# Kernel optimization log

Measured on AMD Instinct MI355X. Metric: run time of the kernel, lower is better.

Reference implementation:

```python
import jax, jax.numpy as jnp
import numpy as np

DIM = 64
HEADS = 4
N_NODES = 50000
N_EDGES = 800000
NEG_SLOPE = 0.2


def setup_inputs() -> dict:
    key = jax.random.key(0)
    k1, k2, k3, k4, k5 = jax.random.split(key, 5)
    meta_x = jax.random.normal(k1, (N_NODES, DIM), dtype=jnp.float32)
    meta_edge_index = jax.random.randint(k2, (2, N_EDGES), 0, N_NODES, dtype=jnp.int64)
    # GATConv params: shared source/dest Linear (no bias), per-head attention vecs, output bias.
    glorot = float(np.sqrt(2.0 / (DIM + HEADS * DIM)))
    W = jax.random.normal(k3, (DIM, HEADS * DIM), dtype=jnp.float32) * glorot  # x @ W
    att_src = jax.random.normal(k4, (1, HEADS, DIM), dtype=jnp.float32) * glorot
    att_dst = jax.random.normal(k5, (1, HEADS, DIM), dtype=jnp.float32) * glorot
    bias = jnp.zeros((DIM,), dtype=jnp.float32)
    return {"meta_x": meta_x, "meta_edge_index": meta_edge_index,
            "W": W, "att_src": att_src, "att_dst": att_dst, "bias": bias}


def reference(meta_x, meta_edge_index, W, att_src, att_dst, bias):
    N = meta_x.shape[0]
    # PyG GATConv default: add self-loops
    loops = jnp.arange(N, dtype=meta_edge_index.dtype)
    edge = jnp.concatenate([meta_edge_index, jnp.stack([loops, loops])], axis=1)
    src, dst = edge[0], edge[1]

    x = (meta_x @ W).reshape(N, HEADS, DIM)            # [N, H, C]
    a_src = jnp.sum(x * att_src, axis=-1)              # [N, H]
    a_dst = jnp.sum(x * att_dst, axis=-1)              # [N, H]

    logits = a_src[src] + a_dst[dst]                   # [E, H]
    logits = jax.nn.leaky_relu(logits, NEG_SLOPE)

    # segment softmax over edges grouped by destination node
    seg_max = jax.ops.segment_max(logits, dst, num_segments=N)   # [N, H]
    ex = jnp.exp(logits - seg_max[dst])
    seg_sum = jax.ops.segment_sum(ex, dst, num_segments=N)
    alpha = ex / (seg_sum[dst] + 1e-16)                # [E, H]

    msg = x[src] * alpha[:, :, None]                   # [E, H, C]
    out = jax.ops.segment_sum(msg, dst, num_segments=N)  # [N, H, C]
    # concat=False -> mean over heads, then bias
    return out.mean(axis=1) + bias
```

## Files before the change

kernel.cpp:

```cpp
#include <hip/hip_runtime.h>
#include <hip/hip_bf16.h>
#include <math.h>

#define MAXDEG 64

__device__ __forceinline__ float lrelu(float v) { return v > 0.0f ? v : 0.2f * v; }

__global__ void prep_kernel(int4* __restrict__ cnt4, int n4,
                            const float* __restrict__ W, const float* __restrict__ att_src,
                            const float* __restrict__ att_dst, float* __restrict__ wsrc,
                            float* __restrict__ wdst) {
  int idx = blockIdx.x * 256 + threadIdx.x;
  for (int i = idx; i < n4; i += gridDim.x * 256) cnt4[i] = make_int4(0, 0, 0, 0);
  if (blockIdx.x == 0) {
    int t = threadIdx.x;
    int h = t >> 6, k = t & 63;
    const float* wrow = W + (size_t)k * 256 + h * 64;
    const float* as = att_src + h * 64;
    const float* ad = att_dst + h * 64;
    float ss = 0.f, sd = 0.f;
#pragma unroll
    for (int c = 0; c < 64; ++c) {
      float w = wrow[c];
      ss = fmaf(w, as[c], ss);
      sd = fmaf(w, ad[c], sd);
    }
    wsrc[k * 4 + h] = ss;
    wdst[k * 4 + h] = sd;
  }
}

__global__ void nh_kernel(const float* __restrict__ x, const float4* __restrict__ wsrc4,
                          const float4* __restrict__ wdst4, float4* __restrict__ asrc4,
                          float4* __restrict__ adst4, __hip_bfloat16* __restrict__ xh,
                          const int* __restrict__ ei, int* __restrict__ counts,
                          int E, int N, int nbh) {
  if (blockIdx.x < nbh) {
    int i = blockIdx.x * 256 + threadIdx.x;
    int E4 = E >> 2;
    if (i < E4) {
      int4 d = ((const int4*)(ei + E))[i];
      atomicAdd(&counts[d.x], 1);
      atomicAdd(&counts[d.y], 1);
      atomicAdd(&counts[d.z], 1);
      atomicAdd(&counts[d.w], 1);
    } else if (i < E4 + N) {
      atomicAdd(&counts[i - E4], 1);
    }
    return;
  }
  int lane = threadIdx.x & 63;
  int n = (blockIdx.x - nbh) * 4 + (threadIdx.x >> 6);
  if (n >= N) return;
  float xv = x[(size_t)n * 64 + lane];
  xh[(size_t)n * 64 + lane] = __float2bfloat16(xv);
  float4 ws = wsrc4[lane], wd = wdst4[lane];
  float s0 = xv * ws.x, s1 = xv * ws.y, s2 = xv * ws.z, s3 = xv * ws.w;
  float d0 = xv * wd.x, d1 = xv * wd.y, d2 = xv * wd.z, d3 = xv * wd.w;
#pragma unroll
  for (int m = 1; m < 64; m <<= 1) {
    s0 += __shfl_xor(s0, m, 64); s1 += __shfl_xor(s1, m, 64);
    s2 += __shfl_xor(s2, m, 64); s3 += __shfl_xor(s3, m, 64);
    d0 += __shfl_xor(d0, m, 64); d1 += __shfl_xor(d1, m, 64);
    d2 += __shfl_xor(d2, m, 64); d3 += __shfl_xor(d3, m, 64);
  }
  if (lane == 0) {
    asrc4[n] = make_float4(s0, s1, s2, s3);
    adst4[n] = make_float4(d0, d1, d2, d3);
  }
}

__global__ void nattn_kernel(const float* __restrict__ x, const float4* __restrict__ wsrc4,
                             const float4* __restrict__ wdst4, float4* __restrict__ asrc4,
                             float4* __restrict__ adst4, __hip_bfloat16* __restrict__ xh,
                             int N) {
  int lane = threadIdx.x & 63;
  int n = blockIdx.x * 4 + (threadIdx.x >> 6);
  if (n >= N) return;
  float xv = x[(size_t)n * 64 + lane];
  xh[(size_t)n * 64 + lane] = __float2bfloat16(xv);
  float4 ws = wsrc4[lane], wd = wdst4[lane];
  float s0 = xv * ws.x, s1 = xv * ws.y, s2 = xv * ws.z, s3 = xv * ws.w;
  float d0 = xv * wd.x, d1 = xv * wd.y, d2 = xv * wd.z, d3 = xv * wd.w;
#pragma unroll
  for (int m = 1; m < 64; m <<= 1) {
    s0 += __shfl_xor(s0, m, 64); s1 += __shfl_xor(s1, m, 64);
    s2 += __shfl_xor(s2, m, 64); s3 += __shfl_xor(s3, m, 64);
    d0 += __shfl_xor(d0, m, 64); d1 += __shfl_xor(d1, m, 64);
    d2 += __shfl_xor(d2, m, 64); d3 += __shfl_xor(d3, m, 64);
  }
  if (lane == 0) {
    asrc4[n] = make_float4(s0, s1, s2, s3);
    adst4[n] = make_float4(d0, d1, d2, d3);
  }
}

__global__ void hist_kernel(const int* __restrict__ ei, int* __restrict__ counts,
                            int E, int N) {
  int e = blockIdx.x * 256 + threadIdx.x;
  int ET = E + N;
  if (e >= ET) return;
  int dst = (e < E) ? ei[(size_t)E + e] : (e - E);
  atomicAdd(&counts[dst], 1);
}

__global__ void scatter_kernel(const int* __restrict__ ei, int* __restrict__ cursor,
                               int* __restrict__ src_sorted, int E, int N) {
  int e = blockIdx.x * 256 + threadIdx.x;
  int ET = E + N;
  if (e >= ET) return;
  int src, dst;
  if (e < E) {
    src = ei[e];
    dst = ei[(size_t)E + e];
  } else {
    src = dst = e - E;
  }
  int pos = atomicAdd(&cursor[dst], 1);
  src_sorted[pos] = src;
}

__global__ void scatter8_kernel(const int* __restrict__ ei, int* __restrict__ cursor,
                                int* __restrict__ srt, int E, int N) {
  int slice = blockIdx.x & 7;
  int bid = blockIdx.x >> 3;
  int nb = gridDim.x >> 3;
  int chunk = (N + 7) >> 3;
  int lo = slice * chunk;
  int hi = lo + chunk; if (hi > N) hi = N;
  int E4 = E >> 2;
  const int4* s4p = (const int4*)ei;
  const int4* d4p = (const int4*)(ei + E);
  int stride = nb * 256;
  for (int i = bid * 256 + threadIdx.x; i < E4; i += stride) {
    int4 d4 = d4p[i];
    bool bx = (d4.x >= lo && d4.x < hi), by = (d4.y >= lo && d4.y < hi);
    bool bz = (d4.z >= lo && d4.z < hi), bw = (d4.w >= lo && d4.w < hi);
    if (!(bx || by || bz || bw)) continue;
    int4 s4 = s4p[i];
    if (bx) { int p = atomicAdd(&cursor[d4.x], 1); srt[p] = s4.x; }
    if (by) { int p = atomicAdd(&cursor[d4.y], 1); srt[p] = s4.y; }
    if (bz) { int p = atomicAdd(&cursor[d4.z], 1); srt[p] = s4.z; }
    if (bw) { int p = atomicAdd(&cursor[d4.w], 1); srt[p] = s4.w; }
  }
  for (int n = lo + bid * 256 + threadIdx.x; n < hi; n += stride) {
    int p = atomicAdd(&cursor[n], 1);
    srt[p] = n;
  }
}

__global__ void scanABC_kernel(const int* __restrict__ cnt, int* __restrict__ row,
                               int* __restrict__ cur, int N, int ntiles) {
  __shared__ int tl[256];
  __shared__ int part[256];
  int b = blockIdx.x, t = threadIdx.x;
  int s = 0;
  if (t < ntiles) {
    const int4* c4 = (const int4*)cnt + t * 64;
    for (int i = 0; i < 64; ++i) {
      int4 v = c4[i];
      s += v.x + v.y + v.z + v.w;
    }
  }
  tl[t] = s;
  __syncthreads();
  for (int d = 1; d < 256; d <<= 1) {
    int u = (t >= d) ? tl[t - d] : 0;
    __syncthreads();
    tl[t] += u;
    __syncthreads();
  }
  int tileoff = (b == 0) ? 0 : tl[b - 1];
  int idx = b * 256 + t;
  int c = (idx < N) ? cnt[idx] : 0;
  part[t] = c;
  __syncthreads();
  for (int d = 1; d < 256; d <<= 1) {
    int u = (t >= d) ? part[t - d] : 0;
    __syncthreads();
    part[t] += u;
    __syncthreads();
  }
  int exc = part[t] - c + tileoff;
  if (idx < N) {
    row[idx] = exc;
    cur[idx] = exc;
    if (idx == N - 1) row[N] = exc + c;
  }
}

__global__ void scanA_kernel(const int* __restrict__ cnt, int* __restrict__ tsum, int N) {
  int b = blockIdx.x, t = threadIdx.x;
  int idx = b * 256 + t;
  int v = (idx < N) ? cnt[idx] : 0;
#pragma unroll
  for (int m = 1; m < 64; m <<= 1) v += __shfl_xor(v, m, 64);
  __shared__ int ws[4];
  if ((t & 63) == 0) ws[t >> 6] = v;
  __syncthreads();
  if (t == 0) tsum[b] = ws[0] + ws[1] + ws[2] + ws[3];
}

__global__ void scanB_kernel(int* __restrict__ tsum, int ntiles) {
  __shared__ int part[256];
  int t = threadIdx.x;
  int carry = 0;
  for (int b0 = 0; b0 < ntiles; b0 += 256) {
    int idx = b0 + t;
    int v = (idx < ntiles) ? tsum[idx] : 0;
    part[t] = v;
    __syncthreads();
    for (int d = 1; d < 256; d <<= 1) {
      int u = (t >= d) ? part[t - d] : 0;
      __syncthreads();
      part[t] += u;
      __syncthreads();
    }
    if (idx < ntiles) tsum[idx] = part[t] - v + carry;
    carry += part[255];
    __syncthreads();
  }
}

__global__ void scanC_kernel(const int* __restrict__ cnt, const int* __restrict__ tsum,
                             int* __restrict__ row, int* __restrict__ cur, int N) {
  __shared__ int part[256];
  int b = blockIdx.x, t = threadIdx.x;
  int idx = b * 256 + t;
  int c = (idx < N) ? cnt[idx] : 0;
  part[t] = c;
  __syncthreads();
  for (int d = 1; d < 256; d <<= 1) {
    int u = (t >= d) ? part[t - d] : 0;
    __syncthreads();
    part[t] += u;
    __syncthreads();
  }
  int exc = part[t] - c + tsum[b];
  if (idx < N) {
    row[idx] = exc;
    cur[idx] = exc;
    if (idx == N - 1) row[N] = exc + c;
  }
}

__global__ __launch_bounds__(256) void agg_kernel(
    const int* __restrict__ srt, const int* __restrict__ row,
    const float4* __restrict__ asrc4, const float4* __restrict__ adst4,
    const __hip_bfloat16* __restrict__ xh, __hip_bfloat16* __restrict__ agg, int N) {
  __shared__ float4 alL[4][MAXDEG];
  __shared__ int slL[4][MAXDEG];
  int t = threadIdx.x, w = t >> 6, lane = t & 63;
  int n = blockIdx.x * 4 + w;
  if (n >= N) return;
  int start = row[n], end = row[n + 1];
  int deg = end - start;
  float4 ad = adst4[n];
  float t0 = 0.f, t1 = 0.f, t2 = 0.f, t3 = 0.f;
  if (deg <= MAXDEG) {
    for (int b = 0; b < deg; b += 64) {
      if (b + lane < deg) {
        int sl = srt[start + b + lane];
        float4 as = asrc4[sl];
        float4 e;
        e.x = __expf(lrelu(as.x + ad.x));
        e.y = __expf(lrelu(as.y + ad.y));
        e.z = __expf(lrelu(as.z + ad.z));
        e.w = __expf(lrelu(as.w + ad.w));
        alL[w][b + lane] = e;
        slL[w][b + lane] = sl;
        t0 += e.x; t1 += e.y; t2 += e.z; t3 += e.w;
      }
    }
  } else {
    for (int b = start; b < end; b += 64) {
      int idx = b + lane;
      if (idx < end) {
        int sl = srt[idx];
        float4 as = asrc4[sl];
        t0 += __expf(lrelu(as.x + ad.x));
        t1 += __expf(lrelu(as.y + ad.y));
        t2 += __expf(lrelu(as.z + ad.z));
        t3 += __expf(lrelu(as.w + ad.w));
      }
    }
  }
#pragma unroll
  for (int m = 1; m < 64; m <<= 1) {
    t0 += __shfl_xor(t0, m, 64);
    t1 += __shfl_xor(t1, m, 64);
    t2 += __shfl_xor(t2, m, 64);
    t3 += __shfl_xor(t3, m, 64);
  }
  float r0 = 0.25f / (t0 + 1e-16f), r1 = 0.25f / (t1 + 1e-16f);
  float r2 = 0.25f / (t2 + 1e-16f), r3 = 0.25f / (t3 + 1e-16f);
  float a0 = 0.f, a1 = 0.f, a2 = 0.f, a3 = 0.f;
  if (deg <= MAXDEG) {
    int j = 0;
    for (; j + 4 <= deg; j += 4) {
      float4 e0 = alL[w][j], e1 = alL[w][j + 1], e2 = alL[w][j + 2], e3 = alL[w][j + 3];
      int q0 = slL[w][j], q1 = slL[w][j + 1], q2 = slL[w][j + 2], q3 = slL[w][j + 3];
      float v0 = __bfloat162float(xh[(size_t)q0 * 64 + lane]);
      float v1 = __bfloat162float(xh[(size_t)q1 * 64 + lane]);
      float v2 = __bfloat162float(xh[(size_t)q2 * 64 + lane]);
      float v3 = __bfloat162float(xh[(size_t)q3 * 64 + lane]);
      a0 = fmaf(e0.x, v0, a0); a1 = fmaf(e0.y, v0, a1);
      a2 = fmaf(e0.z, v0, a2); a3 = fmaf(e0.w, v0, a3);
      a0 = fmaf(e1.x, v1, a0); a1 = fmaf(e1.y, v1, a1);
      a2 = fmaf(e1.z, v1, a2); a3 = fmaf(e1.w, v1, a3);
      a0 = fmaf(e2.x, v2, a0); a1 = fmaf(e2.y, v2, a1);
      a2 = fmaf(e2.z, v2, a2); a3 = fmaf(e2.w, v2, a3);
      a0 = fmaf(e3.x, v3, a0); a1 = fmaf(e3.y, v3, a1);
      a2 = fmaf(e3.z, v3, a2); a3 = fmaf(e3.w, v3, a3);
    }
    for (; j < deg; ++j) {
      float4 e0 = alL[w][j];
      int q0 = slL[w][j];
      float v0 = __bfloat162float(xh[(size_t)q0 * 64 + lane]);
      a0 = fmaf(e0.x, v0, a0); a1 = fmaf(e0.y, v0, a1);
      a2 = fmaf(e0.z, v0, a2); a3 = fmaf(e0.w, v0, a3);
    }
  } else {
    for (int b = start; b < end; b += 64) {
      int cnt = end - b;
      if (cnt > 64) cnt = 64;
      int idx = b + lane;
      int sl = 0;
      float e0 = 0.f, e1 = 0.f, e2 = 0.f, e3 = 0.f;
      if (idx < end) {
        sl = srt[idx];
        float4 as = asrc4[sl];
        e0 = __expf(lrelu(as.x + ad.x));
        e1 = __expf(lrelu(as.y + ad.y));
        e2 = __expf(lrelu(as.z + ad.z));
        e3 = __expf(lrelu(as.w + ad.w));
      }
      for (int j = 0; j < cnt; ++j) {
        int sj = __shfl(sl, j, 64);
        float b0 = __shfl(e0, j, 64), b1 = __shfl(e1, j, 64);
        float b2 = __shfl(e2, j, 64), b3 = __shfl(e3, j, 64);
        float v = __bfloat162float(xh[(size_t)sj * 64 + lane]);
        a0 = fmaf(b0, v, a0); a1 = fmaf(b1, v, a1);
        a2 = fmaf(b2, v, a2); a3 = fmaf(b3, v, a3);
      }
    }
  }
  __hip_bfloat16* ao = agg + (size_t)n * 256;
  ao[lane] = __float2bfloat16(a0 * r0);
  ao[64 + lane] = __float2bfloat16(a1 * r1);
  ao[128 + lane] = __float2bfloat16(a2 * r2);
  ao[192 + lane] = __float2bfloat16(a3 * r3);
}

__global__ __launch_bounds__(256) void proj_kernel(
    const __hip_bfloat16* __restrict__ agg, const float* __restrict__ W,
    const float* __restrict__ bias, float* __restrict__ out, int N) {
  __shared__ float aggL[4][256];
  __shared__ float pL[4][4][64];
  int t = threadIdx.x, w = t >> 6, lane = t & 63;
  float Wreg[64];
#pragma unroll
  for (int k = 0; k < 64; ++k) Wreg[k] = W[(size_t)k * 256 + w * 64 + lane];
  float bv = bias[lane];
  int ngroups = (N + 3) >> 2;
  for (int g = blockIdx.x; g < ngroups; g += gridDim.x) {
    int n0 = g * 4;
    __syncthreads();
    {
      int nn = n0 + w;
      if (nn < N) {
        ushort4 u = ((const ushort4*)(agg + (size_t)nn * 256))[t & 63];
        float4 f;
        f.x = __bfloat162float(*(__hip_bfloat16*)&u.x);
        f.y = __bfloat162float(*(__hip_bfloat16*)&u.y);
        f.z = __bfloat162float(*(__hip_bfloat16*)&u.z);
        f.w = __bfloat162float(*(__hip_bfloat16*)&u.w);
        *(float4*)&aggL[w][(t & 63) * 4] = f;
      } else {
        *(float4*)&aggL[w][(t & 63) * 4] = make_float4(0.f, 0.f, 0.f, 0.f);
      }
    }
    __syncthreads();
    float acc0 = 0.f, acc1 = 0.f, acc2 = 0.f, acc3 = 0.f;
#pragma unroll
    for (int k4 = 0; k4 < 16; ++k4) {
      float4 av0 = *(const float4*)&aggL[0][w * 64 + k4 * 4];
      float4 av1 = *(const float4*)&aggL[1][w * 64 + k4 * 4];
      float4 av2 = *(const float4*)&aggL[2][w * 64 + k4 * 4];
      float4 av3 = *(const float4*)&aggL[3][w * 64 + k4 * 4];
      float w0 = Wreg[k4 * 4 + 0], w1 = Wreg[k4 * 4 + 1];
      float w2 = Wreg[k4 * 4 + 2], w3 = Wreg[k4 * 4 + 3];
      acc0 = fmaf(av0.x, w0, acc0); acc0 = fmaf(av0.y, w1, acc0);
      acc0 = fmaf(av0.z, w2, acc0); acc0 = fmaf(av0.w, w3, acc0);
      acc1 = fmaf(av1.x, w0, acc1); acc1 = fmaf(av1.y, w1, acc1);
      acc1 = fmaf(av1.z, w2, acc1); acc1 = fmaf(av1.w, w3, acc1);
      acc2 = fmaf(av2.x, w0, acc2); acc2 = fmaf(av2.y, w1, acc2);
      acc2 = fmaf(av2.z, w2, acc2); acc2 = fmaf(av2.w, w3, acc2);
      acc3 = fmaf(av3.x, w0, acc3); acc3 = fmaf(av3.y, w1, acc3);
      acc3 = fmaf(av3.z, w2, acc3); acc3 = fmaf(av3.w, w3, acc3);
    }
    pL[w][0][lane] = acc0;
    pL[w][1][lane] = acc1;
    pL[w][2][lane] = acc2;
    pL[w][3][lane] = acc3;
    __syncthreads();
    int nn = n0 + w;
    if (nn < N) {
      out[(size_t)nn * 64 + lane] = pL[0][w][lane] + pL[1][w][lane] +
                                    pL[2][w][lane] + pL[3][w][lane] + bv;
    }
  }
}

extern "C" void kernel_launch(void* const* d_in, const int* in_sizes, int n_in,
                              void* d_out, int out_size, void* d_ws, size_t ws_size,
                              hipStream_t stream) {
  const float* meta_x = (const float*)d_in[0];
  const int* ei = (const int*)d_in[1];
  const float* W = (const float*)d_in[2];
  const float* att_src = (const float*)d_in[3];
  const float* att_dst = (const float*)d_in[4];
  const float* bias = (const float*)d_in[5];
  float* out = (float*)d_out;

  int N = in_sizes[0] / 64;
  int E = in_sizes[1] / 2;
  int ET = E + N;
  int ntiles = (N + 255) / 256;

  char* ws = (char*)d_ws;
  size_t off = 0;
  auto alloc = [&](size_t bytes) {
    size_t o = off;
    off += (bytes + 255) & ~(size_t)255;
    return o;
  };
  size_t o_wsrc = alloc(64 * 4 * sizeof(float));
  size_t o_wdst = alloc(64 * 4 * sizeof(float));
  size_t o_asrc = alloc((size_t)N * 4 * sizeof(float));
  size_t o_adst = alloc((size_t)N * 4 * sizeof(float));
  size_t o_cnt = alloc((size_t)ntiles * 256 * sizeof(int));
  size_t o_row = alloc(((size_t)N + 1) * sizeof(int));
  size_t o_cur = alloc((size_t)N * sizeof(int));
  size_t o_srt = alloc((size_t)ET * sizeof(int));
  size_t o_ts = alloc((size_t)ntiles * sizeof(int));
  size_t o_xh = alloc((size_t)N * 64 * sizeof(__hip_bfloat16));
  size_t o_agg = alloc((size_t)N * 256 * sizeof(__hip_bfloat16));
  bool split = (ws_size >= off);
  (void)split;

  float* wsrc = (float*)(ws + o_wsrc);
  float* wdst = (float*)(ws + o_wdst);
  float4* asrc4 = (float4*)(ws + o_asrc);
  float4* adst4 = (float4*)(ws + o_adst);
  int* cnt = (int*)(ws + o_cnt);
  int* row = (int*)(ws + o_row);
  int* cur = (int*)(ws + o_cur);
  int* srt = (int*)(ws + o_srt);
  int* tsum = (int*)(ws + o_ts);
  __hip_bfloat16* xh = (__hip_bfloat16*)(ws + o_xh);
  __hip_bfloat16* aggp = (__hip_bfloat16*)(ws + o_agg);

  int n4 = ntiles * 64;
  prep_kernel<<<64, 256, 0, stream>>>((int4*)cnt, n4, W, att_src, att_dst, wsrc, wdst);

  if ((E & 3) == 0) {
    int nbh = ((E >> 2) + N + 255) / 256;
    int nbn = (N + 3) / 4;
    nh_kernel<<<nbh + nbn, 256, 0, stream>>>(meta_x, (const float4*)wsrc,
                                             (const float4*)wdst, asrc4, adst4, xh,
                                             ei, cnt, E, N, nbh);
  } else {
    nattn_kernel<<<(N + 3) / 4, 256, 0, stream>>>(meta_x, (const float4*)wsrc,
                                                  (const float4*)wdst, asrc4, adst4, xh, N);
    hist_kernel<<<(ET + 255) / 256, 256, 0, stream>>>(ei, cnt, E, N);
  }

  if (ntiles <= 256) {
    scanABC_kernel<<<ntiles, 256, 0, stream>>>(cnt, row, cur, N, ntiles);
  } else {
    scanA_kernel<<<ntiles, 256, 0, stream>>>(cnt, tsum, N);
    scanB_kernel<<<1, 256, 0, stream>>>(tsum, ntiles);
    scanC_kernel<<<ntiles, 256, 0, stream>>>(cnt, tsum, row, cur, N);
  }

  if ((E & 3) == 0) {
    scatter8_kernel<<<2048, 256, 0, stream>>>(ei, cur, srt, E, N);
  } else {
    scatter_kernel<<<(ET + 255) / 256, 256, 0, stream>>>(ei, cur, srt, E, N);
  }

  agg_kernel<<<(N + 3) / 4, 256, 0, stream>>>(srt, row, asrc4, adst4, xh, aggp, N);
  int ngroups = (N + 3) / 4;
  int pgrid = ngroups < 1024 ? ngroups : 1024;
  proj_kernel<<<pgrid, 256, 0, stream>>>(aggp, W, bias, out, N);
}
```

Measured before the change: 185.6 us.

## Partition degree histogram atomics by destination range and preseed self-loop counts

New measurement: 188.5 us. No clear change (+1.5%).

```diff
diff --git a/kernel.cpp b/kernel.cpp
--- a/kernel.cpp
+++ b/kernel.cpp
@@ -6,12 +6,20 @@
 
 __device__ __forceinline__ float lrelu(float v) { return v > 0.0f ? v : 0.2f * v; }
 
-__global__ void prep_kernel(int4* __restrict__ cnt4, int n4,
+__global__ void prep_kernel(int4* __restrict__ cnt4, int n4, int N,
                             const float* __restrict__ W, const float* __restrict__ att_src,
                             const float* __restrict__ att_dst, float* __restrict__ wsrc,
                             float* __restrict__ wdst) {
   int idx = blockIdx.x * 256 + threadIdx.x;
-  for (int i = idx; i < n4; i += gridDim.x * 256) cnt4[i] = make_int4(0, 0, 0, 0);
+  for (int i = idx; i < n4; i += gridDim.x * 256) {
+    int base = i * 4;
+    int4 v;
+    v.x = (base < N) ? 1 : 0;
+    v.y = (base + 1 < N) ? 1 : 0;
+    v.z = (base + 2 < N) ? 1 : 0;
+    v.w = (base + 3 < N) ? 1 : 0;
+    cnt4[i] = v;
+  }
   if (blockIdx.x == 0) {
     int t = threadIdx.x;
     int h = t >> 6, k = t & 63;
@@ -36,16 +44,21 @@
                           const int* __restrict__ ei, int* __restrict__ counts,
                           int E, int N, int nbh) {
   if (blockIdx.x < nbh) {
-    int i = blockIdx.x * 256 + threadIdx.x;
+    int slice = blockIdx.x & 7;
+    int bid = blockIdx.x >> 3;
+    int nb = nbh >> 3;
+    int chunk = (N + 7) >> 3;
+    int lo = slice * chunk;
+    int hi = lo + chunk; if (hi > N) hi = N;
     int E4 = E >> 2;
-    if (i < E4) {
-      int4 d = ((const int4*)(ei + E))[i];
-      atomicAdd(&counts[d.x], 1);
-      atomicAdd(&counts[d.y], 1);
-      atomicAdd(&counts[d.z], 1);
-      atomicAdd(&counts[d.w], 1);
-    } else if (i < E4 + N) {
-      atomicAdd(&counts[i - E4], 1);
+    const int4* d4p = (const int4*)(ei + E);
+    int stride = nb * 256;
+    for (int i = bid * 256 + threadIdx.x; i < E4; i += stride) {
+      int4 d = d4p[i];
+      if (d.x >= lo && d.x < hi) atomicAdd(&counts[d.x], 1);
+      if (d.y >= lo && d.y < hi) atomicAdd(&counts[d.y], 1);
+      if (d.z >= lo && d.z < hi) atomicAdd(&counts[d.z], 1);
+      if (d.w >= lo && d.w < hi) atomicAdd(&counts[d.w], 1);
     }
     return;
   }
@@ -95,13 +108,10 @@
   }
 }
 
-__global__ void hist_kernel(const int* __restrict__ ei, int* __restrict__ counts,
-                            int E, int N) {
+__global__ void hist_kernel(const int* __restrict__ ei, int* __restrict__ counts, int E) {
   int e = blockIdx.x * 256 + threadIdx.x;
-  int ET = E + N;
-  if (e >= ET) return;
-  int dst = (e < E) ? ei[(size_t)E + e] : (e - E);
-  atomicAdd(&counts[dst], 1);
+  if (e >= E) return;
+  atomicAdd(&counts[ei[(size_t)E + e]], 1);
 }
 
 __global__ void scatter_kernel(const int* __restrict__ ei, int* __restrict__ cursor,
@@ -446,8 +456,7 @@
   size_t o_ts = alloc((size_t)ntiles * sizeof(int));
   size_t o_xh = alloc((size_t)N * 64 * sizeof(__hip_bfloat16));
   size_t o_agg = alloc((size_t)N * 256 * sizeof(__hip_bfloat16));
-  bool split = (ws_size >= off);
-  (void)split;
+  (void)ws_size;
 
   float* wsrc = (float*)(ws + o_wsrc);
   float* wdst = (float*)(ws + o_wdst);
@@ -462,10 +471,10 @@
   __hip_bfloat16* aggp = (__hip_bfloat16*)(ws + o_agg);
 
   int n4 = ntiles * 64;
-  prep_kernel<<<64, 256, 0, stream>>>((int4*)cnt, n4, W, att_src, att_dst, wsrc, wdst);
+  prep_kernel<<<64, 256, 0, stream>>>((int4*)cnt, n4, N, W, att_src, att_dst, wsrc, wdst);
 
   if ((E & 3) == 0) {
-    int nbh = ((E >> 2) + N + 255) / 256;
+    int nbh = 2048;
     int nbn = (N + 3) / 4;
     nh_kernel<<<nbh + nbn, 256, 0, stream>>>(meta_x, (const float4*)wsrc,
                                              (const float4*)wdst, asrc4, adst4, xh,
@@ -473,7 +482,7 @@
   } else {
     nattn_kernel<<<(N + 3) / 4, 256, 0, stream>>>(meta_x, (const float4*)wsrc,
                                                   (const float4*)wdst, asrc4, adst4, xh, N);
-    hist_kernel<<<(ET + 255) / 256, 256, 0, stream>>>(ei, cnt, E, N);
+    hist_kernel<<<(E + 255) / 256, 256, 0, stream>>>(ei, cnt, E);
   }
 
   if (ntiles <= 256) {
```
